# Kernel tuning notes

Measured on AMD Instinct MI355X. Metric: run time of the kernel, lower is better.

## Reference

```python
import jax, jax.numpy as jnp
import numpy as np

TAU = 2.0        # spikingjelly LIFNode default tau
ALPHA = 4.0      # sigmoid surrogate alpha (spikingjelly default)
NUM_HEADS = 8
CHUNK = 2

@jax.custom_vjp
def heaviside(x):
    return (x >= 0).astype(x.dtype)

def _h_fwd(x):
    return heaviside(x), x

def _h_bwd(x, g):
    s = jax.nn.sigmoid(ALPHA * x)
    return (g * ALPHA * s * (1.0 - s),)

heaviside.defvjp(_h_fwd, _h_bwd)

def lif(x, v_th):
    # multi-step LIF: v <- v + (x - v)/tau ; spike = H(v - v_th) ; hard reset to 0
    def step(v, xt):
        v = v + (xt - v) / TAU
        s = heaviside(v - v_th)
        return v * (1.0 - s), s
    _, spikes = jax.lax.scan(step, jnp.zeros_like(x[0]), x)
    return spikes

def bn(x, p, eps=1e-5):
    # eval-mode BatchNorm1d over channel dim C of [T,B,C,V]; p = [gamma,beta,mean,var] each [C]
    g, b, m, v = p[0], p[1], p[2], p[3]
    scale = g * jax.lax.rsqrt(v + eps)
    return (x - m[:, None]) * scale[:, None] + b[:, None]

def setup_inputs() -> dict:
    key = jax.random.key(0)
    T, B, C, V = 8, 16, 256, 1024
    ks = jax.random.split(key, 10)
    def mk_bn(k):
        k1, k2, k3, k4 = jax.random.split(k, 4)
        return jnp.stack([
            jax.random.uniform(k1, (C,)) + 0.5,          # gamma
            0.1 * jax.random.normal(k2, (C,)),           # beta
            0.1 * jax.random.normal(k3, (C,)),           # running mean
            jax.random.uniform(k4, (C,)) * 0.5 + 0.5,    # running var (>0)
        ])
    w_scale = C ** -0.5
    return {
        "x": jax.random.normal(ks[0], (T, B, C, V), jnp.float32),
        "q_w": w_scale * jax.random.normal(ks[1], (C, C), jnp.float32),
        "k_w": w_scale * jax.random.normal(ks[2], (C, C), jnp.float32),
        "v_w": w_scale * jax.random.normal(ks[3], (C, C), jnp.float32),
        "proj_w": w_scale * jax.random.normal(ks[4], (C, C), jnp.float32),
        "proj_b": 0.01 * jax.random.normal(ks[5], (C,), jnp.float32),
        "bn_q": mk_bn(ks[6]),
        "bn_k": mk_bn(ks[7]),
        "bn_v": mk_bn(ks[8]),
        "bn_proj": mk_bn(ks[9]),
    }

def reference(x, q_w, k_w, v_w, proj_w, proj_b, bn_q, bn_k, bn_v, bn_proj):
    T, B, C, V = x.shape
    H = NUM_HEADS
    D = C // H
    N = V
    NC = T // CHUNK
    identity = x

    xs = lif(x, 1.0)  # shortcut_lif

    def branch(w, bnp):
        y = jnp.einsum('oc,tbcv->tbov', w, xs)   # 1x1 conv
        y = lif(bn(y, bnp), 1.0)
        # [T,B,C,V] -> [T,B,H,N,D]
        return y.transpose(0, 1, 3, 2).reshape(T, B, N, H, D).transpose(0, 1, 3, 2, 4)

    q = branch(q_w, bn_q)
    k = branch(k_w, bn_k)
    v = branch(v_w, bn_v)

    def chunk(t):
        # [T,B,H,N,D] -> [NC,B,H,CHUNK*N,D]
        return (t.reshape(NC, CHUNK, B, H, N, D)
                 .transpose(0, 2, 3, 1, 4, 5)
                 .reshape(NC, B, H, CHUNK * N, D))

    qc, kc, vc = chunk(q), chunk(k), chunk(v)
    attn = jnp.einsum('nbhld,nbhle->nbhde', kc, vc) * (1.0 / N)  # [NC,B,H,D,D]
    out = jnp.einsum('nbhld,nbhde->nbhle', qc, attn)             # [NC,B,H,CHUNK*N,D]
    out = (out.reshape(NC, B, H, CHUNK, N, D)
              .transpose(0, 3, 1, 2, 4, 5)
              .reshape(T, B, H, N, D))

    y = out.transpose(0, 1, 2, 4, 3).reshape(T, B, C, N)  # [T,B,H,D,N] -> [T,B,C,N]
    y = lif(y, 0.5)  # attn_lif
    y = jnp.einsum('oc,tbcv->tbov', proj_w, y) + proj_b[None, None, :, None]
    y = bn(y, bn_proj)
    return y + identity, v
```

## Files before the change

### kernel.cpp

```cpp
#include <hip/hip_runtime.h>
#include <hip/hip_bf16.h>
#include <math.h>

typedef __bf16 bf16_t;
typedef __bf16 bf16x8 __attribute__((ext_vector_type(8)));
typedef __bf16 bf16x4 __attribute__((ext_vector_type(4)));
typedef float  f32x4  __attribute__((ext_vector_type(4)));

#define T_ 8
#define B_ 16
#define C_ 256
#define V_ 1024
#define H_ 8
#define D_ 32

#define MFMA __builtin_amdgcn_mfma_f32_16x16x32_bf16

__global__ __launch_bounds__(256) void k0_split4(const float* __restrict__ W0,
                                                 const float* __restrict__ W1,
                                                 const float* __restrict__ W2,
                                                 const float* __restrict__ W3,
                                                 bf16_t* __restrict__ S)
{
    const int mat = blockIdx.x >> 6;
    const float* W = (mat == 0) ? W0 : (mat == 1) ? W1 : (mat == 2) ? W2 : W3;
    bf16_t* S0 = S + (size_t)mat * 3 * 65536;
    bf16_t* S1 = S0 + 65536;
    bf16_t* S2 = S0 + 131072;
    int i = ((blockIdx.x & 63) * 256 + threadIdx.x) * 4;
    float4 w = *(const float4*)(W + i);
    float wv[4] = {w.x, w.y, w.z, w.w};
    bf16x4 s0, s1, s2;
#pragma unroll
    for (int j = 0; j < 4; j++) {
        bf16_t a = (bf16_t)wv[j];
        float r1 = wv[j] - (float)a;
        bf16_t b = (bf16_t)r1;
        float r2 = r1 - (float)b;
        bf16_t c = (bf16_t)r2;
        s0[j] = a; s1[j] = b; s2[j] = c;
    }
    *(bf16x4*)(S0 + i) = s0;
    *(bf16x4*)(S1 + i) = s1;
    *(bf16x4*)(S2 + i) = s2;
}

__global__ __launch_bounds__(256) void k1_lif_tr(const float* __restrict__ x,
                                                 bf16_t* __restrict__ xsT)
{
    __shared__ bf16_t tile[64 * 72];
    const int v0 = blockIdx.x * 64, c0 = blockIdx.y * 64, b = blockIdx.z;
    const int tid = threadIdx.x;
    const int cc = tid >> 2, v16 = (tid & 3) * 16;
    const int vr = tid >> 2, c16 = (tid & 3) * 16;
    float mem[16];
#pragma unroll
    for (int j = 0; j < 16; j++) mem[j] = 0.0f;

    for (int t = 0; t < T_; t++) {
        const float* xp = x + (((size_t)(t * B_ + b) * C_ + (c0 + cc)) * V_ + v0 + v16);
        float xv[16];
#pragma unroll
        for (int q = 0; q < 4; q++) {
            float4 f = *(const float4*)(xp + q * 4);
            xv[q * 4 + 0] = f.x; xv[q * 4 + 1] = f.y;
            xv[q * 4 + 2] = f.z; xv[q * 4 + 3] = f.w;
        }
#pragma unroll
        for (int j = 0; j < 16; j++) {
            float m = mem[j];
            float d = xv[j] - m;
            m = m + d * 0.5f;
            float s = (m >= 1.0f) ? 1.0f : 0.0f;
            tile[(v16 + j) * 72 + cc] = (bf16_t)s;
            mem[j] = (s != 0.0f) ? 0.0f : m;
        }
        __syncthreads();
        bf16_t* op = xsT + (((size_t)(t * B_ + b) * V_ + (v0 + vr)) * C_ + c0 + c16);
        *(bf16x8*)op       = *(const bf16x8*)&tile[vr * 72 + c16];
        *(bf16x8*)(op + 8) = *(const bf16x8*)&tile[vr * 72 + c16 + 8];
        __syncthreads();
    }
}

template <int ORIENT, int VOUT>
__global__ __launch_bounds__(256, 2) void k_branch(const bf16_t* __restrict__ Wsp,
                                                   const float* __restrict__ bnp,
                                                   const bf16_t* __restrict__ xsT,
                                                   bf16_t* __restrict__ outp, float vth,
                                                   float* __restrict__ out1)
{
    __shared__ bf16_t Wl[3][64 * 40];
    __shared__ bf16_t Xl[8][64 * 40];
    __shared__ float bsc[64], bmn[64], bbt[64];
    const int v0 = blockIdx.x * 64, o0 = blockIdx.y * 64, b = blockIdx.z;
    const int tid = threadIdx.x;
    const int w = tid >> 6, l = tid & 63, lq = l >> 4, lr = l & 15;
    const int msub = (w >> 1) * 32, nsub = (w & 1) * 32;

    if (tid < 64) {
        int o = o0 + tid;
        float g = bnp[o], be = bnp[C_ + o];
        float mn = bnp[2 * C_ + o], vr2 = bnp[3 * C_ + o];
        bsc[tid] = g * (1.0f / sqrtf(vr2 + 1e-5f));
        bmn[tid] = mn; bbt[tid] = be;
    }

    f32x4 acc[8][4];
#pragma unroll
    for (int t = 0; t < 8; t++)
#pragma unroll
        for (int i = 0; i < 4; i++) acc[t][i] = (f32x4){0.f, 0.f, 0.f, 0.f};

    bf16x8 wst[3], xst[8];
#pragma unroll
    for (int i = 0; i < 3; i++) {
        int ch = tid + i * 256, lvl = ch >> 8, rem = ch & 255;
        int row = rem >> 2, col8 = (rem & 3) * 8;
        wst[i] = *(const bf16x8*)&Wsp[lvl * 65536 + (o0 + row) * 256 + col8];
    }
#pragma unroll
    for (int i = 0; i < 8; i++) {
        int ch = tid + i * 256, tt = ch >> 8, rem = ch & 255;
        int row = rem >> 2, col8 = (rem & 3) * 8;
        xst[i] = *(const bf16x8*)&xsT[((size_t)(tt * B_ + b) * V_ + v0 + row) * C_ + col8];
    }

    for (int kq = 0; kq < 8; kq++) {
        __syncthreads();
#pragma unroll
        for (int i = 0; i < 3; i++) {
            int ch = tid + i * 256, lvl = ch >> 8, rem = ch & 255;
            int row = rem >> 2, col8 = (rem & 3) * 8;
            *(bf16x8*)&Wl[lvl][row * 40 + col8] = wst[i];
        }
#pragma unroll
        for (int i = 0; i < 8; i++) {
            int ch = tid + i * 256, tt = ch >> 8, rem = ch & 255;
            int row = rem >> 2, col8 = (rem & 3) * 8;
            *(bf16x8*)&Xl[tt][row * 40 + col8] = xst[i];
        }
        __syncthreads();
        if (kq < 7) {
            int kc8 = (kq + 1) * 32;
#pragma unroll
            for (int i = 0; i < 3; i++) {
                int ch = tid + i * 256, lvl = ch >> 8, rem = ch & 255;
                int row = rem >> 2, col8 = (rem & 3) * 8;
                wst[i] = *(const bf16x8*)&Wsp[lvl * 65536 + (o0 + row) * 256 + kc8 + col8];
            }
#pragma unroll
            for (int i = 0; i < 8; i++) {
                int ch = tid + i * 256, tt = ch >> 8, rem = ch & 255;
                int row = rem >> 2, col8 = (rem & 3) * 8;
                xst[i] = *(const bf16x8*)&xsT[((size_t)(tt * B_ + b) * V_ + v0 + row) * C_ + kc8 + col8];
            }
        }

        bf16x8 aw0[3], aw1[3];
#pragma unroll
        for (int lvl = 0; lvl < 3; lvl++) {
            aw0[lvl] = *(const bf16x8*)&Wl[lvl][(msub + lr) * 40 + lq * 8];
            aw1[lvl] = *(const bf16x8*)&Wl[lvl][(msub + 16 + lr) * 40 + lq * 8];
        }
#pragma unroll
        for (int t = 0; t < 8; t++) {
            bf16x8 b0 = *(const bf16x8*)&Xl[t][(nsub + lr) * 40 + lq * 8];
            bf16x8 b1 = *(const bf16x8*)&Xl[t][(nsub + 16 + lr) * 40 + lq * 8];
#pragma unroll
            for (int lvl = 0; lvl < 3; lvl++) {
                if (ORIENT == 0) {
                    acc[t][0] = MFMA(aw0[lvl], b0, acc[t][0], 0, 0, 0);
                    acc[t][1] = MFMA(aw0[lvl], b1, acc[t][1], 0, 0, 0);
                    acc[t][2] = MFMA(aw1[lvl], b0, acc[t][2], 0, 0, 0);
                    acc[t][3] = MFMA(aw1[lvl], b1, acc[t][3], 0, 0, 0);
                } else {
                    acc[t][0] = MFMA(b0, aw0[lvl], acc[t][0], 0, 0, 0);
                    acc[t][1] = MFMA(b1, aw0[lvl], acc[t][1], 0, 0, 0);
                    acc[t][2] = MFMA(b0, aw1[lvl], acc[t][2], 0, 0, 0);
                    acc[t][3] = MFMA(b1, aw1[lvl], acc[t][3], 0, 0, 0);
                }
            }
        }
    }

    bf16_t* tl = (bf16_t*)Xl;
    if (VOUT) __syncthreads();
    float mem[4][4];
#pragma unroll
    for (int st = 0; st < 4; st++)
#pragma unroll
        for (int r = 0; r < 4; r++) mem[st][r] = 0.0f;
#pragma unroll
    for (int t = 0; t < 8; t++) {
#pragma unroll
        for (int st = 0; st < 4; st++) {
            int mi = st >> 1, ni = st & 1;
#pragma unroll
            for (int r = 0; r < 4; r++) {
                int m, n;
                if (ORIENT == 0) {
                    m = msub + mi * 16 + lq * 4 + r;
                    n = nsub + ni * 16 + lr;
                } else {
                    m = msub + mi * 16 + lr;
                    n = nsub + ni * 16 + lq * 4 + r;
                }
                float y = (acc[t][st][r] - bmn[m]) * bsc[m] + bbt[m];
                float mm = mem[st][r];
                mm = mm + (y - mm) * 0.5f;
                float s = (mm >= vth) ? 1.0f : 0.0f;
                size_t idx = ORIENT
                    ? (((size_t)(t * B_ + b) * V_ + (v0 + n)) * C_ + (o0 + m))
                    : (((size_t)(t * B_ + b) * C_ + (o0 + m)) * V_ + (v0 + n));
                outp[idx] = (bf16_t)s;
                mem[st][r] = (s != 0.0f) ? 0.0f : mm;
                if (VOUT) tl[n * 66 + m] = (bf16_t)s;
            }
        }
        if (VOUT) {
            __syncthreads();
            int nn = tid & 63, ho = tid >> 6;
            int h = (o0 >> 5) + (ho >> 1), d16 = (ho & 1) * 16;
            float* op = out1 + ((size_t)((t * B_ + b) * H_ + h)) * (V_ * D_)
                             + (size_t)(v0 + nn) * D_ + d16;
#pragma unroll
            for (int q2 = 0; q2 < 4; q2++) {
                float4 o4;
                o4.x = (float)tl[nn * 66 + ho * 16 + q2 * 4 + 0];
                o4.y = (float)tl[nn * 66 + ho * 16 + q2 * 4 + 1];
                o4.z = (float)tl[nn * 66 + ho * 16 + q2 * 4 + 2];
                o4.w = (float)tl[nn * 66 + ho * 16 + q2 * 4 + 3];
                *(float4*)(op + q2 * 4) = o4;
            }
            __syncthreads();
        }
    }
}

__global__ __launch_bounds__(256) void k_attn(const bf16_t* __restrict__ vc,
                                              const bf16_t* __restrict__ kc,
                                              bf16_t* __restrict__ ahi,
                                              bf16_t* __restrict__ alo)
{
    __shared__ float red[3][64][20];
    const int fid = blockIdx.x;
    const int h = fid & 7, b = (fid >> 3) & 15, nc = fid >> 7;
    const int tid = threadIdx.x, w = tid >> 6, l = tid & 63, lq = l >> 4, lr = l & 15;
    f32x4 acc[4];
#pragma unroll
    for (int i = 0; i < 4; i++) acc[i] = (f32x4){0.f, 0.f, 0.f, 0.f};
    for (int ss = 0; ss < 16; ss++) {
        int s = w * 16 + ss;
        int t = nc * 2 + (s >> 5);
        int n0 = (s & 31) * 32;
        size_t rb = ((size_t)(t * B_ + b) * C_ + h * D_ + lr) * V_ + n0 + lq * 8;
        bf16x8 a0 = *(const bf16x8*)&vc[rb];
        bf16x8 a1 = *(const bf16x8*)&vc[rb + (size_t)16 * V_];
        bf16x8 b0 = *(const bf16x8*)&kc[rb];
        bf16x8 b1 = *(const bf16x8*)&kc[rb + (size_t)16 * V_];
        acc[0] = MFMA(a0, b0, acc[0], 0, 0, 0);
        acc[1] = MFMA(a0, b1, acc[1], 0, 0, 0);
        acc[2] = MFMA(a1, b0, acc[2], 0, 0, 0);
        acc[3] = MFMA(a1, b1, acc[3], 0, 0, 0);
    }
    if (w) {
#pragma unroll
        for (int st = 0; st < 4; st++)
            *(f32x4*)&red[w - 1][l][st * 4] = acc[st];
    }
    __syncthreads();
    if (w == 0) {
#pragma unroll
        for (int st = 0; st < 4; st++)
#pragma unroll
            for (int i = 0; i < 3; i++)
                acc[st] += *(const f32x4*)&red[i][l][st * 4];

        size_t ob = (size_t)fid * 1024;
#pragma unroll
        for (int st = 0; st < 4; st++) {
            int ei = st >> 1, di = st & 1;
#pragma unroll
            for (int r = 0; r < 4; r++) {
                int e = ei * 16 + lq * 4 + r;
                int d = di * 16 + lr;
                float val = acc[st][r] * (1.0f / 1024.0f);
                bf16_t hi = (bf16_t)val;
                float lo = val - (float)hi;
                ahi[ob + e * 32 + d] = hi;
                alo[ob + e * 32 + d] = (bf16_t)lo;
            }
        }
    }
}

__global__ __launch_bounds__(256) void k_attn_out(const bf16_t* __restrict__ qT,
                                                  const bf16_t* __restrict__ ahi,
                                                  const bf16_t* __restrict__ alo,
                                                  bf16_t* __restrict__ y3T)
{
    const int tid = threadIdx.x, w = tid >> 6, l = tid & 63, lq = l >> 4, lr = l & 15;
    const int n0 = blockIdx.x * 64 + (w >> 1) * 32;
    const int h = blockIdx.y * 2 + (w & 1);
    const int b = blockIdx.z;
    float mem[4][4];
#pragma unroll
    for (int st = 0; st < 4; st++)
#pragma unroll
        for (int r = 0; r < 4; r++) mem[st][r] = 0.0f;

    for (int t = 0; t < T_; t++) {
        int nc = t >> 1;
        const bf16_t* qp = qT + ((size_t)(t * B_ + b) * V_ + n0 + lr) * C_ + h * D_ + lq * 8;
        bf16x8 a0 = *(const bf16x8*)qp;
        bf16x8 a1 = *(const bf16x8*)(qp + 16 * C_);
        size_t ab = ((size_t)(nc * B_ + b) * H_ + h) * 1024;
        bf16x8 bh0 = *(const bf16x8*)&ahi[ab + lr * 32 + lq * 8];
        bf16x8 bh1 = *(const bf16x8*)&ahi[ab + (16 + lr) * 32 + lq * 8];
        bf16x8 bl0 = *(const bf16x8*)&alo[ab + lr * 32 + lq * 8];
        bf16x8 bl1 = *(const bf16x8*)&alo[ab + (16 + lr) * 32 + lq * 8];
#pragma unroll
        for (int st = 0; st < 4; st++) {
            int mi = st >> 1, ni = st & 1;
            f32x4 z = (f32x4){0.f, 0.f, 0.f, 0.f};
            z = MFMA(mi ? a1 : a0, ni ? bh1 : bh0, z, 0, 0, 0);
            z = MFMA(mi ? a1 : a0, ni ? bl1 : bl0, z, 0, 0, 0);
#pragma unroll
            for (int r = 0; r < 4; r++) {
                int n = n0 + mi * 16 + lq * 4 + r;
                int e = ni * 16 + lr;
                float mm = mem[st][r];
                mm = mm + (z[r] - mm) * 0.5f;
                float s = (mm >= 0.5f) ? 1.0f : 0.0f;
                y3T[((size_t)(t * B_ + b) * V_ + n) * C_ + h * D_ + e] = (bf16_t)s;
                mem[st][r] = (s != 0.0f) ? 0.0f : mm;
            }
        }
    }
}

__global__ __launch_bounds__(256, 2) void k_proj(const bf16_t* __restrict__ Wsp,
                                                 const float* __restrict__ pb,
                                                 const float* __restrict__ bnp,
                                                 const bf16_t* __restrict__ y3T,
                                                 const float* __restrict__ x,
                                                 float* __restrict__ out0)
{
    __shared__ bf16_t Wl[3][64 * 40];
    __shared__ bf16_t Xl[8][64 * 40];
    __shared__ float bsc[64], bmn[64], bbt[64], bbi[64];
    const int v0 = blockIdx.x * 64, o0 = blockIdx.y * 64, b = blockIdx.z;
    const int tid = threadIdx.x;
    const int w = tid >> 6, l = tid & 63, lq = l >> 4, lr = l & 15;
    const int msub = (w >> 1) * 32, nsub = (w & 1) * 32;

    if (tid < 64) {
        int o = o0 + tid;
        float g = bnp[o], be = bnp[C_ + o];
        float mn = bnp[2 * C_ + o], vr2 = bnp[3 * C_ + o];
        bsc[tid] = g * (1.0f / sqrtf(vr2 + 1e-5f));
        bmn[tid] = mn; bbt[tid] = be; bbi[tid] = pb[o];
    }

    f32x4 acc[8][4];
#pragma unroll
    for (int t = 0; t < 8; t++)
#pragma unroll
        for (int i = 0; i < 4; i++) acc[t][i] = (f32x4){0.f, 0.f, 0.f, 0.f};

    bf16x8 wst[3], xst[8];
#pragma unroll
    for (int i = 0; i < 3; i++) {
        int ch = tid + i * 256, lvl = ch >> 8, rem = ch & 255;
        int row = rem >> 2, col8 = (rem & 3) * 8;
        wst[i] = *(const bf16x8*)&Wsp[lvl * 65536 + (o0 + row) * 256 + col8];
    }
#pragma unroll
    for (int i = 0; i < 8; i++) {
        int ch = tid + i * 256, tt = ch >> 8, rem = ch & 255;
        int row = rem >> 2, col8 = (rem & 3) * 8;
        xst[i] = *(const bf16x8*)&y3T[((size_t)(tt * B_ + b) * V_ + v0 + row) * C_ + col8];
    }

    for (int kq = 0; kq < 8; kq++) {
        __syncthreads();
#pragma unroll
        for (int i = 0; i < 3; i++) {
            int ch = tid + i * 256, lvl = ch >> 8, rem = ch & 255;
            int row = rem >> 2, col8 = (rem & 3) * 8;
            *(bf16x8*)&Wl[lvl][row * 40 + col8] = wst[i];
        }
#pragma unroll
        for (int i = 0; i < 8; i++) {
            int ch = tid + i * 256, tt = ch >> 8, rem = ch & 255;
            int row = rem >> 2, col8 = (rem & 3) * 8;
            *(bf16x8*)&Xl[tt][row * 40 + col8] = xst[i];
        }
        __syncthreads();
        if (kq < 7) {
            int kc8 = (kq + 1) * 32;
#pragma unroll
            for (int i = 0; i < 3; i++) {
                int ch = tid + i * 256, lvl = ch >> 8, rem = ch & 255;
                int row = rem >> 2, col8 = (rem & 3) * 8;
                wst[i] = *(const bf16x8*)&Wsp[lvl * 65536 + (o0 + row) * 256 + kc8 + col8];
            }
#pragma unroll
            for (int i = 0; i < 8; i++) {
                int ch = tid + i * 256, tt = ch >> 8, rem = ch & 255;
                int row = rem >> 2, col8 = (rem & 3) * 8;
                xst[i] = *(const bf16x8*)&y3T[((size_t)(tt * B_ + b) * V_ + v0 + row) * C_ + kc8 + col8];
            }
        }

        bf16x8 aw0[3], aw1[3];
#pragma unroll
        for (int lvl = 0; lvl < 3; lvl++) {
            aw0[lvl] = *(const bf16x8*)&Wl[lvl][(msub + lr) * 40 + lq * 8];
            aw1[lvl] = *(const bf16x8*)&Wl[lvl][(msub + 16 + lr) * 40 + lq * 8];
        }
#pragma unroll
        for (int t = 0; t < 8; t++) {
            bf16x8 b0 = *(const bf16x8*)&Xl[t][(nsub + lr) * 40 + lq * 8];
            bf16x8 b1 = *(const bf16x8*)&Xl[t][(nsub + 16 + lr) * 40 + lq * 8];
#pragma unroll
            for (int lvl = 0; lvl < 3; lvl++) {
                acc[t][0] = MFMA(aw0[lvl], b0, acc[t][0], 0, 0, 0);
                acc[t][1] = MFMA(aw0[lvl], b1, acc[t][1], 0, 0, 0);
                acc[t][2] = MFMA(aw1[lvl], b0, acc[t][2], 0, 0, 0);
                acc[t][3] = MFMA(aw1[lvl], b1, acc[t][3], 0, 0, 0);
            }
        }
    }

#pragma unroll
    for (int t = 0; t < 8; t++) {
#pragma unroll
        for (int st = 0; st < 4; st++) {
            int mi = st >> 1, ni = st & 1;
#pragma unroll
            for (int r = 0; r < 4; r++) {
                int m = msub + mi * 16 + lq * 4 + r;
                int n = nsub + ni * 16 + lr;
                size_t idx = ((size_t)(t * B_ + b) * C_ + (o0 + m)) * V_ + (v0 + n);
                float y = acc[t][st][r] + bbi[m];
                y = (y - bmn[m]) * bsc[m] + bbt[m];
                y += x[idx];
                out0[idx] = y;
            }
        }
    }
}

extern "C" void kernel_launch(void* const* d_in, const int* in_sizes, int n_in,
                              void* d_out, int out_size, void* d_ws, size_t ws_size,
                              hipStream_t stream)
{
    const float* x    = (const float*)d_in[0];
    const float* q_w  = (const float*)d_in[1];
    const float* k_w  = (const float*)d_in[2];
    const float* v_w  = (const float*)d_in[3];
    const float* pw   = (const float*)d_in[4];
    const float* pb   = (const float*)d_in[5];
    const float* bn_q = (const float*)d_in[6];
    const float* bn_k = (const float*)d_in[7];
    const float* bn_v = (const float*)d_in[8];
    const float* bn_p = (const float*)d_in[9];

    char* ws = (char*)d_ws;
    bf16_t* xsT  = (bf16_t*)(ws);
    bf16_t* vc   = (bf16_t*)(ws + ((size_t)64 << 20));
    bf16_t* ahi  = (bf16_t*)(ws + ((size_t)128 << 20));
    bf16_t* alo  = (bf16_t*)(ws + ((size_t)129 << 20));
    bf16_t* wspq = (bf16_t*)(ws + ((size_t)130 << 20));
    bf16_t* wspk = wspq + 3 * 65536;
    bf16_t* wspv = wspk + 3 * 65536;
    bf16_t* wspp = wspv + 3 * 65536;
    bf16_t* y3T  = xsT;

    float* outf = (float*)d_out;
    float* out1 = outf + (size_t)33554432;
    bf16_t* qT = (bf16_t*)d_out;
    bf16_t* kc = (bf16_t*)((char*)d_out + ((size_t)64 << 20));

    k0_split4   <<<dim3(256),       256, 0, stream>>>(q_w, k_w, v_w, pw, wspq);
    k1_lif_tr   <<<dim3(16, 4, 16), 256, 0, stream>>>(x, xsT);
    k_branch<1,0><<<dim3(16, 4, 16),256, 0, stream>>>(wspq, bn_q, xsT, qT, 1.0f, nullptr);
    k_branch<0,0><<<dim3(16, 4, 16),256, 0, stream>>>(wspk, bn_k, xsT, kc, 1.0f, nullptr);
    k_branch<0,1><<<dim3(16, 4, 16),256, 0, stream>>>(wspv, bn_v, xsT, vc, 1.0f, out1);
    k_attn      <<<dim3(512),       256, 0, stream>>>(vc, kc, ahi, alo);
    k_attn_out  <<<dim3(16, 4, 16), 256, 0, stream>>>(qT, ahi, alo, y3T);
    k_proj      <<<dim3(16, 4, 16), 256, 0, stream>>>(wspp, pb, bn_p, y3T, x, outf);
}
```

Measured before the change: 764.1 us.

## Use direct global-to-LDS loads with K-chunked blocked layouts for GEMM operands

Result: slower. 1.258 ms (+64.7%).

```diff
diff --git a/kernel.cpp b/kernel.cpp
--- a/kernel.cpp
+++ b/kernel.cpp
@@ -16,6 +16,14 @@
 
 #define MFMA __builtin_amdgcn_mfma_f32_16x16x32_bf16
 
+__device__ __forceinline__ void gload16(const bf16_t* g, bf16_t* l)
+{
+    __builtin_amdgcn_global_load_lds(
+        (const __attribute__((address_space(1))) unsigned int*)(g),
+        (__attribute__((address_space(3))) unsigned int*)(l), 16, 0, 0);
+}
+
+
 __global__ __launch_bounds__(256) void k0_split4(const float* __restrict__ W0,
                                                  const float* __restrict__ W1,
                                                  const float* __restrict__ W2,
@@ -24,11 +32,11 @@
 {
     const int mat = blockIdx.x >> 6;
     const float* W = (mat == 0) ? W0 : (mat == 1) ? W1 : (mat == 2) ? W2 : W3;
-    bf16_t* S0 = S + (size_t)mat * 3 * 65536;
-    bf16_t* S1 = S0 + 65536;
-    bf16_t* S2 = S0 + 131072;
-    int i = ((blockIdx.x & 63) * 256 + threadIdx.x) * 4;
-    float4 w = *(const float4*)(W + i);
+    bf16_t* Sm = S + (size_t)mat * 3 * 65536;
+    int f = ((blockIdx.x & 63) * 256 + threadIdx.x) * 4;
+    int o = f >> 8, c = f & 255;
+    int kq = c >> 5, kk = c & 31;
+    float4 w = *(const float4*)(W + f);
     float wv[4] = {w.x, w.y, w.z, w.w};
     bf16x4 s0, s1, s2;
 #pragma unroll
@@ -37,12 +45,13 @@
         float r1 = wv[j] - (float)a;
         bf16_t b = (bf16_t)r1;
         float r2 = r1 - (float)b;
-        bf16_t c = (bf16_t)r2;
-        s0[j] = a; s1[j] = b; s2[j] = c;
-    }
-    *(bf16x4*)(S0 + i) = s0;
-    *(bf16x4*)(S1 + i) = s1;
-    *(bf16x4*)(S2 + i) = s2;
+        bf16_t c2 = (bf16_t)r2;
+        s0[j] = a; s1[j] = b; s2[j] = c2;
+    }
+    size_t base = (size_t)kq * 8192 + o * 32 + kk;
+    *(bf16x4*)(Sm + base)          = s0;
+    *(bf16x4*)(Sm + 65536 + base)  = s1;
+    *(bf16x4*)(Sm + 131072 + base) = s2;
 }
 
 __global__ __launch_bounds__(256) void k1_lif_tr(const float* __restrict__ x,
@@ -76,7 +85,9 @@
             mem[j] = (s != 0.0f) ? 0.0f : m;
         }
         __syncthreads();
-        bf16_t* op = xsT + (((size_t)(t * B_ + b) * V_ + (v0 + vr)) * C_ + c0 + c16);
+        int c_abs = c0 + c16;
+        bf16_t* op = xsT + ((((size_t)(t * B_ + b) * 8) + (c_abs >> 5)) * 1024 + (v0 + vr)) * 32
+                         + (c_abs & 31);
         *(bf16x8*)op       = *(const bf16x8*)&tile[vr * 72 + c16];
         *(bf16x8*)(op + 8) = *(const bf16x8*)&tile[vr * 72 + c16 + 8];
         __syncthreads();
@@ -84,19 +95,20 @@
 }
 
 template <int ORIENT, int VOUT>
-__global__ __launch_bounds__(256, 2) void k_branch(const bf16_t* __restrict__ Wsp,
+__global__ __launch_bounds__(256, 3) void k_branch(const bf16_t* __restrict__ Wsp,
                                                    const float* __restrict__ bnp,
                                                    const bf16_t* __restrict__ xsT,
                                                    bf16_t* __restrict__ outp, float vth,
                                                    float* __restrict__ out1)
 {
-    __shared__ bf16_t Wl[3][64 * 40];
-    __shared__ bf16_t Xl[8][64 * 40];
+    __shared__ bf16_t Wl[3][2048];
+    __shared__ bf16_t Xl[8][2048];
     __shared__ float bsc[64], bmn[64], bbt[64];
     const int v0 = blockIdx.x * 64, o0 = blockIdx.y * 64, b = blockIdx.z;
     const int tid = threadIdx.x;
     const int w = tid >> 6, l = tid & 63, lq = l >> 4, lr = l & 15;
     const int msub = (w >> 1) * 32, nsub = (w & 1) * 32;
+    const int srow = tid >> 2, sc16 = (tid & 3) * 8;
 
     if (tid < 64) {
         int o = o0 + tid;
@@ -112,61 +124,28 @@
 #pragma unroll
         for (int i = 0; i < 4; i++) acc[t][i] = (f32x4){0.f, 0.f, 0.f, 0.f};
 
-    bf16x8 wst[3], xst[8];
-#pragma unroll
-    for (int i = 0; i < 3; i++) {
-        int ch = tid + i * 256, lvl = ch >> 8, rem = ch & 255;
-        int row = rem >> 2, col8 = (rem & 3) * 8;
-        wst[i] = *(const bf16x8*)&Wsp[lvl * 65536 + (o0 + row) * 256 + col8];
-    }
-#pragma unroll
-    for (int i = 0; i < 8; i++) {
-        int ch = tid + i * 256, tt = ch >> 8, rem = ch & 255;
-        int row = rem >> 2, col8 = (rem & 3) * 8;
-        xst[i] = *(const bf16x8*)&xsT[((size_t)(tt * B_ + b) * V_ + v0 + row) * C_ + col8];
-    }
-
     for (int kq = 0; kq < 8; kq++) {
         __syncthreads();
 #pragma unroll
-        for (int i = 0; i < 3; i++) {
-            int ch = tid + i * 256, lvl = ch >> 8, rem = ch & 255;
-            int row = rem >> 2, col8 = (rem & 3) * 8;
-            *(bf16x8*)&Wl[lvl][row * 40 + col8] = wst[i];
-        }
-#pragma unroll
-        for (int i = 0; i < 8; i++) {
-            int ch = tid + i * 256, tt = ch >> 8, rem = ch & 255;
-            int row = rem >> 2, col8 = (rem & 3) * 8;
-            *(bf16x8*)&Xl[tt][row * 40 + col8] = xst[i];
-        }
-        __syncthreads();
-        if (kq < 7) {
-            int kc8 = (kq + 1) * 32;
-#pragma unroll
-            for (int i = 0; i < 3; i++) {
-                int ch = tid + i * 256, lvl = ch >> 8, rem = ch & 255;
-                int row = rem >> 2, col8 = (rem & 3) * 8;
-                wst[i] = *(const bf16x8*)&Wsp[lvl * 65536 + (o0 + row) * 256 + kc8 + col8];
-            }
-#pragma unroll
-            for (int i = 0; i < 8; i++) {
-                int ch = tid + i * 256, tt = ch >> 8, rem = ch & 255;
-                int row = rem >> 2, col8 = (rem & 3) * 8;
-                xst[i] = *(const bf16x8*)&xsT[((size_t)(tt * B_ + b) * V_ + v0 + row) * C_ + kc8 + col8];
-            }
-        }
+        for (int lvl = 0; lvl < 3; lvl++)
+            gload16(&Wsp[(size_t)(lvl * 8 + kq) * 8192 + (o0 + srow) * 32 + sc16],
+                    &Wl[lvl][tid * 8]);
+#pragma unroll
+        for (int tt = 0; tt < 8; tt++)
+            gload16(&xsT[((((size_t)(tt * B_ + b) * 8) + kq) * 1024 + v0 + srow) * 32 + sc16],
+                    &Xl[tt][tid * 8]);
+        __syncthreads();
 
         bf16x8 aw0[3], aw1[3];
 #pragma unroll
         for (int lvl = 0; lvl < 3; lvl++) {
-            aw0[lvl] = *(const bf16x8*)&Wl[lvl][(msub + lr) * 40 + lq * 8];
-            aw1[lvl] = *(const bf16x8*)&Wl[lvl][(msub + 16 + lr) * 40 + lq * 8];
+            aw0[lvl] = *(const bf16x8*)&Wl[lvl][(msub + lr) * 32 + lq * 8];
+            aw1[lvl] = *(const bf16x8*)&Wl[lvl][(msub + 16 + lr) * 32 + lq * 8];
         }
 #pragma unroll
         for (int t = 0; t < 8; t++) {
-            bf16x8 b0 = *(const bf16x8*)&Xl[t][(nsub + lr) * 40 + lq * 8];
-            bf16x8 b1 = *(const bf16x8*)&Xl[t][(nsub + 16 + lr) * 40 + lq * 8];
+            bf16x8 b0 = *(const bf16x8*)&Xl[t][(nsub + lr) * 32 + lq * 8];
+            bf16x8 b1 = *(const bf16x8*)&Xl[t][(nsub + 16 + lr) * 32 + lq * 8];
 #pragma unroll
             for (int lvl = 0; lvl < 3; lvl++) {
                 if (ORIENT == 0) {
@@ -210,9 +189,14 @@
                 float mm = mem[st][r];
                 mm = mm + (y - mm) * 0.5f;
                 float s = (mm >= vth) ? 1.0f : 0.0f;
-                size_t idx = ORIENT
-                    ? (((size_t)(t * B_ + b) * V_ + (v0 + n)) * C_ + (o0 + m))
-                    : (((size_t)(t * B_ + b) * C_ + (o0 + m)) * V_ + (v0 + n));
+                size_t idx;
+                if (ORIENT == 0) {
+                    idx = ((size_t)(t * B_ + b) * C_ + (o0 + m)) * V_ + (v0 + n);
+                } else {
+                    int o_abs = o0 + m;
+                    idx = ((((size_t)(t * B_ + b) * 8) + (o_abs >> 5)) * 1024 + (v0 + n)) * 32
+                        + (o_abs & 31);
+                }
                 outp[idx] = (bf16_t)s;
                 mem[st][r] = (s != 0.0f) ? 0.0f : mm;
                 if (VOUT) tl[n * 66 + m] = (bf16_t)s;
@@ -312,9 +296,9 @@
 
     for (int t = 0; t < T_; t++) {
         int nc = t >> 1;
-        const bf16_t* qp = qT + ((size_t)(t * B_ + b) * V_ + n0 + lr) * C_ + h * D_ + lq * 8;
-        bf16x8 a0 = *(const bf16x8*)qp;
-        bf16x8 a1 = *(const bf16x8*)(qp + 16 * C_);
+        size_t qb = (((size_t)(t * B_ + b) * 8) + h) * 32768;
+        bf16x8 a0 = *(const bf16x8*)&qT[qb + (n0 + lr) * 32 + lq * 8];
+        bf16x8 a1 = *(const bf16x8*)&qT[qb + (n0 + 16 + lr) * 32 + lq * 8];
         size_t ab = ((size_t)(nc * B_ + b) * H_ + h) * 1024;
         bf16x8 bh0 = *(const bf16x8*)&ahi[ab + lr * 32 + lq * 8];
         bf16x8 bh1 = *(const bf16x8*)&ahi[ab + (16 + lr) * 32 + lq * 8];
@@ -333,27 +317,28 @@
                 float mm = mem[st][r];
                 mm = mm + (z[r] - mm) * 0.5f;
                 float s = (mm >= 0.5f) ? 1.0f : 0.0f;
-                y3T[((size_t)(t * B_ + b) * V_ + n) * C_ + h * D_ + e] = (bf16_t)s;
+                y3T[(((size_t)(t * B_ + b) * 8) + h) * 32768 + (size_t)n * 32 + e] = (bf16_t)s;
                 mem[st][r] = (s != 0.0f) ? 0.0f : mm;
             }
         }
     }
 }
 
-__global__ __launch_bounds__(256, 2) void k_proj(const bf16_t* __restrict__ Wsp,
+__global__ __launch_bounds__(256, 3) void k_proj(const bf16_t* __restrict__ Wsp,
                                                  const float* __restrict__ pb,
                                                  const float* __restrict__ bnp,
                                                  const bf16_t* __restrict__ y3T,
                                                  const float* __restrict__ x,
                                                  float* __restrict__ out0)
 {
-    __shared__ bf16_t Wl[3][64 * 40];
-    __shared__ bf16_t Xl[8][64 * 40];
+    __shared__ bf16_t Wl[3][2048];
+    __shared__ bf16_t Xl[8][2048];
     __shared__ float bsc[64], bmn[64], bbt[64], bbi[64];
     const int v0 = blockIdx.x * 64, o0 = blockIdx.y * 64, b = blockIdx.z;
     const int tid = threadIdx.x;
     const int w = tid >> 6, l = tid & 63, lq = l >> 4, lr = l & 15;
     const int msub = (w >> 1) * 32, nsub = (w & 1) * 32;
+    const int srow = tid >> 2, sc16 = (tid & 3) * 8;
 
     if (tid < 64) {
         int o = o0 + tid;
@@ -369,61 +354,28 @@
 #pragma unroll
         for (int i = 0; i < 4; i++) acc[t][i] = (f32x4){0.f, 0.f, 0.f, 0.f};
 
-    bf16x8 wst[3], xst[8];
-#pragma unroll
-    for (int i = 0; i < 3; i++) {
-        int ch = tid + i * 256, lvl = ch >> 8, rem = ch & 255;
-        int row = rem >> 2, col8 = (rem & 3) * 8;
-        wst[i] = *(const bf16x8*)&Wsp[lvl * 65536 + (o0 + row) * 256 + col8];
-    }
-#pragma unroll
-    for (int i = 0; i < 8; i++) {
-        int ch = tid + i * 256, tt = ch >> 8, rem = ch & 255;
-        int row = rem >> 2, col8 = (rem & 3) * 8;
-        xst[i] = *(const bf16x8*)&y3T[((size_t)(tt * B_ + b) * V_ + v0 + row) * C_ + col8];
-    }
-
     for (int kq = 0; kq < 8; kq++) {
         __syncthreads();
 #pragma unroll
-        for (int i = 0; i < 3; i++) {
-            int ch = tid + i * 256, lvl = ch >> 8, rem = ch & 255;
-            int row = rem >> 2, col8 = (rem & 3) * 8;
-            *(bf16x8*)&Wl[lvl][row * 40 + col8] = wst[i];
-        }
-#pragma unroll
-        for (int i = 0; i < 8; i++) {
-            int ch = tid + i * 256, tt = ch >> 8, rem = ch & 255;
-            int row = rem >> 2, col8 = (rem & 3) * 8;
-            *(bf16x8*)&Xl[tt][row * 40 + col8] = xst[i];
-        }
-        __syncthreads();
-        if (kq < 7) {
-            int kc8 = (kq + 1) * 32;
-#pragma unroll
-            for (int i = 0; i < 3; i++) {
-                int ch = tid + i * 256, lvl = ch >> 8, rem = ch & 255;
-                int row = rem >> 2, col8 = (rem & 3) * 8;
-                wst[i] = *(const bf16x8*)&Wsp[lvl * 65536 + (o0 + row) * 256 + kc8 + col8];
-            }
-#pragma unroll
-            for (int i = 0; i < 8; i++) {
-                int ch = tid + i * 256, tt = ch >> 8, rem = ch & 255;
-                int row = rem >> 2, col8 = (rem & 3) * 8;
-                xst[i] = *(const bf16x8*)&y3T[((size_t)(tt * B_ + b) * V_ + v0 + row) * C_ + kc8 + col8];
-            }
-        }
+        for (int lvl = 0; lvl < 3; lvl++)
+            gload16(&Wsp[(size_t)(lvl * 8 + kq) * 8192 + (o0 + srow) * 32 + sc16],
+                    &Wl[lvl][tid * 8]);
+#pragma unroll
+        for (int tt = 0; tt < 8; tt++)
+            gload16(&y3T[((((size_t)(tt * B_ + b) * 8) + kq) * 1024 + v0 + srow) * 32 + sc16],
+                    &Xl[tt][tid * 8]);
+        __syncthreads();
 
         bf16x8 aw0[3], aw1[3];
 #pragma unroll
         for (int lvl = 0; lvl < 3; lvl++) {
-            aw0[lvl] = *(const bf16x8*)&Wl[lvl][(msub + lr) * 40 + lq * 8];
-            aw1[lvl] = *(const bf16x8*)&Wl[lvl][(msub + 16 + lr) * 40 + lq * 8];
+            aw0[lvl] = *(const bf16x8*)&Wl[lvl][(msub + lr) * 32 + lq * 8];
+            aw1[lvl] = *(const bf16x8*)&Wl[lvl][(msub + 16 + lr) * 32 + lq * 8];
         }
 #pragma unroll
         for (int t = 0; t < 8; t++) {
-            bf16x8 b0 = *(const bf16x8*)&Xl[t][(nsub + lr) * 40 + lq * 8];
-            bf16x8 b1 = *(const bf16x8*)&Xl[t][(nsub + 16 + lr) * 40 + lq * 8];
+            bf16x8 b0 = *(const bf16x8*)&Xl[t][(nsub + lr) * 32 + lq * 8];
+            bf16x8 b1 = *(const bf16x8*)&Xl[t][(nsub + 16 + lr) * 32 + lq * 8];
 #pragma unroll
             for (int lvl = 0; lvl < 3; lvl++) {
                 acc[t][0] = MFMA(aw0[lvl], b0, acc[t][0], 0, 0, 0);
```
